# Kernel tuning notes

Hardware: AMD Instinct MI355X
Metric: run time of the kernel (lower is better)

## Reference

```python
import jax, jax.numpy as jnp
import numpy as np

N_NODES = 500_000
N_EDGES = 16_000_000
N_TYPES = 64


def setup_inputs() -> dict:
    key = jax.random.key(0)
    ks = jax.random.split(key, 8)
    voltage = jax.random.normal(ks[0], (N_NODES,), dtype=jnp.float32)
    stimulus = jax.random.normal(ks[1], (N_NODES,), dtype=jnp.float32)
    neuron_type = jax.random.randint(ks[2], (N_NODES,), 0, N_TYPES, dtype=jnp.int64)
    edge_index = jax.random.randint(ks[3], (2, N_EDGES), 0, N_NODES, dtype=jnp.int64)
    w = jax.random.normal(ks[4], (N_EDGES,), dtype=jnp.float32)
    V_i_rest = jax.random.normal(ks[5], (N_NODES,), dtype=jnp.float32)
    # tau must be positive (divisor); shift uniform away from zero
    tau_i = jax.random.uniform(ks[6], (N_NODES,), dtype=jnp.float32) + 0.5
    # multiple_ReLU per-type scale, abs(1 + 0.5*randn) as in the module
    type_params = jnp.abs(1.0 + 0.5 * jax.random.normal(ks[7], (N_TYPES, 1), dtype=jnp.float32))
    return {
        "voltage": voltage,
        "stimulus": stimulus,
        "neuron_type": neuron_type,
        "edge_index": edge_index,
        "w": w,
        "V_i_rest": V_i_rest,
        "tau_i": tau_i,
        "type_params": type_params,
    }


def reference(voltage, stimulus, neuron_type, edge_index, w, V_i_rest, tau_i, type_params):
    # voltage: (N,), edge_index: (2,E), w: (E,), type_params: (T,1)
    v = voltage[:, None]  # (N,1)
    src = edge_index[0]
    dst = edge_index[1]
    # per-edge message: w_e * relu(v_src) * param[type(src)]   -> (E,1)
    edge_msg = w[:, None] * jax.nn.relu(v[src]) * type_params[neuron_type[src]]
    # scatter_add to destination nodes -> (N,1)
    msg = jax.ops.segment_sum(edge_msg, dst, num_segments=v.shape[0])
    # dv/dt = (-v + msg + e + v_rest) / tau
    dv = (-v + msg + stimulus[:, None] + V_i_rest[:, None]) / tau_i[:, None]
    return dv
```

## Files before the change

### kernel.cpp

```cpp
#include <hip/hip_runtime.h>


#define BSHIFT 11
#define BSIZE  2048
#define NBMAX  256
#define GPB    4096
#define EPB    (GPB * 4)
#define EPBP   (EPB + 1024)
#define MAPSZ  (EPBP / 4)
#define SPILL_CAP 131072

__device__ __forceinline__ unsigned pack_rec(float x, int d) {
    return ((__float_as_uint(x) + (unsigned)(BSIZE >> 1)) & ~(unsigned)(BSIZE - 1)) |
           ((unsigned)d & (BSIZE - 1));
}


__global__ void pre_g_kernel(const float* __restrict__ v,
                             const int* __restrict__ ntype,
                             const float* __restrict__ tp,
                             float* __restrict__ g,
                             unsigned* __restrict__ gcur,
                             int n, int nb) {
    int i = blockIdx.x * blockDim.x + threadIdx.x;
    if (i < n) {
        float x = v[i];
        x = x > 0.0f ? x : 0.0f;
        g[i] = x * tp[ntype[i]];
    }
    if (i <= nb) gcur[i] = 0u;
}

__global__ __launch_bounds__(1024, 8)
void scatter_kernel(const int* __restrict__ src,
                    const int* __restrict__ dst,
                    const float* __restrict__ w,
                    const float* __restrict__ g,
                    unsigned* __restrict__ bucketbuf,
                    unsigned* __restrict__ gcur,
                    uint2* __restrict__ spill,
                    int G, int n_edges, int nblk, int nb, int cap) {
    __shared__ unsigned stage[EPBP];
    __shared__ unsigned lstart[NBMAX];
    __shared__ unsigned lcur[NBMAX];
    __shared__ unsigned gposs[NBMAX];
    __shared__ unsigned char qmap[MAPSZ];
    __shared__ unsigned wsum[16];
    int blk = blockIdx.x, tid = threadIdx.x;
    int wid = tid >> 6, lane = tid & 63;
    bool last = (blk == nblk - 1);

    if (tid < NBMAX) lcur[tid] = 0;
    __syncthreads();

    const int4*   s4 = (const int4*)src;
    const int4*   d4 = (const int4*)dst;
    const float4* w4 = (const float4*)w;
    int gstart = blk * GPB;
    int gend = gstart + GPB; if (gend > G) gend = G;
    bool full = (gend - gstart) == GPB;

    int4 dreg[4];
    float4 wreg[4];
    float gv[16];
    if (full) {
        int i0 = gstart + tid;
        int4 dA = d4[i0], dB = d4[i0 + 1024], dC = d4[i0 + 2048], dD = d4[i0 + 3072];
        int4 sA = s4[i0], sB = s4[i0 + 1024], sC = s4[i0 + 2048], sD = s4[i0 + 3072];
        wreg[0] = w4[i0]; wreg[1] = w4[i0 + 1024];
        wreg[2] = w4[i0 + 2048]; wreg[3] = w4[i0 + 3072];
        gv[0]  = g[sA.x]; gv[1]  = g[sA.y]; gv[2]  = g[sA.z]; gv[3]  = g[sA.w];
        gv[4]  = g[sB.x]; gv[5]  = g[sB.y]; gv[6]  = g[sB.z]; gv[7]  = g[sB.w];
        gv[8]  = g[sC.x]; gv[9]  = g[sC.y]; gv[10] = g[sC.z]; gv[11] = g[sC.w];
        gv[12] = g[sD.x]; gv[13] = g[sD.y]; gv[14] = g[sD.z]; gv[15] = g[sD.w];
        dreg[0] = dA; dreg[1] = dB; dreg[2] = dC; dreg[3] = dD;
        atomicAdd(&lcur[((unsigned)dA.x) >> BSHIFT], 1u);
        atomicAdd(&lcur[((unsigned)dA.y) >> BSHIFT], 1u);
        atomicAdd(&lcur[((unsigned)dA.z) >> BSHIFT], 1u);
        atomicAdd(&lcur[((unsigned)dA.w) >> BSHIFT], 1u);
        atomicAdd(&lcur[((unsigned)dB.x) >> BSHIFT], 1u);
        atomicAdd(&lcur[((unsigned)dB.y) >> BSHIFT], 1u);
        atomicAdd(&lcur[((unsigned)dB.z) >> BSHIFT], 1u);
        atomicAdd(&lcur[((unsigned)dB.w) >> BSHIFT], 1u);
        atomicAdd(&lcur[((unsigned)dC.x) >> BSHIFT], 1u);
        atomicAdd(&lcur[((unsigned)dC.y) >> BSHIFT], 1u);
        atomicAdd(&lcur[((unsigned)dC.z) >> BSHIFT], 1u);
        atomicAdd(&lcur[((unsigned)dC.w) >> BSHIFT], 1u);
        atomicAdd(&lcur[((unsigned)dD.x) >> BSHIFT], 1u);
        atomicAdd(&lcur[((unsigned)dD.y) >> BSHIFT], 1u);
        atomicAdd(&lcur[((unsigned)dD.z) >> BSHIFT], 1u);
        atomicAdd(&lcur[((unsigned)dD.w) >> BSHIFT], 1u);
    } else {
        #pragma unroll
        for (int k = 0; k < 4; k++) {
            int i = gstart + tid + k * 1024;
            if (i < gend) {
                int4 d = d4[i];
                dreg[k] = d;
                atomicAdd(&lcur[((unsigned)d.x) >> BSHIFT], 1u);
                atomicAdd(&lcur[((unsigned)d.y) >> BSHIFT], 1u);
                atomicAdd(&lcur[((unsigned)d.z) >> BSHIFT], 1u);
                atomicAdd(&lcur[((unsigned)d.w) >> BSHIFT], 1u);
            }
        }
    }
    if (last) {
        for (int i = G * 4 + tid; i < n_edges; i += 1024)
            atomicAdd(&lcur[((unsigned)dst[i]) >> BSHIFT], 1u);
    }
    __syncthreads();

    unsigned rawc = (tid < NBMAX) ? lcur[tid] : 0u;
    unsigned cntv = (rawc + 3u) & ~3u;
    unsigned inc = cntv;
    #pragma unroll
    for (int o = 1; o < 64; o <<= 1) {
        unsigned t = __shfl_up(inc, o, 64);
        if (lane >= o) inc += t;
    }
    if (lane == 63) wsum[wid] = inc;
    __syncthreads();
    if (tid < 64) {
        unsigned x = (lane < 16) ? wsum[lane] : 0u;
        unsigned xi = x;
        #pragma unroll
        for (int o = 1; o < 16; o <<= 1) {
            unsigned t = __shfl_up(xi, o, 64);
            if (lane >= o) xi += t;
        }
        if (lane < 16) wsum[lane] = xi - x;
    }
    __syncthreads();
    if (tid < NBMAX) {
        unsigned excl = inc - cntv + wsum[wid];
        lstart[tid] = excl;
        lcur[tid] = excl;
    }
    __syncthreads();

    if (full) {
        #pragma unroll
        for (int k = 0; k < 4; k++) {
            float4 wv = wreg[k];
            int4 d = dreg[k];
            unsigned pos;
            pos = atomicAdd(&lcur[((unsigned)d.x) >> BSHIFT], 1u);
            stage[pos] = pack_rec(wv.x * gv[4 * k + 0], d.x);
            pos = atomicAdd(&lcur[((unsigned)d.y) >> BSHIFT], 1u);
            stage[pos] = pack_rec(wv.y * gv[4 * k + 1], d.y);
            pos = atomicAdd(&lcur[((unsigned)d.z) >> BSHIFT], 1u);
            stage[pos] = pack_rec(wv.z * gv[4 * k + 2], d.z);
            pos = atomicAdd(&lcur[((unsigned)d.w) >> BSHIFT], 1u);
            stage[pos] = pack_rec(wv.w * gv[4 * k + 3], d.w);
        }
    } else {
        #pragma unroll
        for (int k = 0; k < 4; k++) {
            int i = gstart + tid + k * 1024;
            if (i < gend) {
                int4 s = s4[i]; float4 wv = w4[i]; int4 d = dreg[k];
                unsigned pos;
                pos = atomicAdd(&lcur[((unsigned)d.x) >> BSHIFT], 1u);
                stage[pos] = pack_rec(wv.x * g[s.x], d.x);
                pos = atomicAdd(&lcur[((unsigned)d.y) >> BSHIFT], 1u);
                stage[pos] = pack_rec(wv.y * g[s.y], d.y);
                pos = atomicAdd(&lcur[((unsigned)d.z) >> BSHIFT], 1u);
                stage[pos] = pack_rec(wv.z * g[s.z], d.z);
                pos = atomicAdd(&lcur[((unsigned)d.w) >> BSHIFT], 1u);
                stage[pos] = pack_rec(wv.w * g[s.w], d.w);
            }
        }
    }
    if (last) {
        for (int i = G * 4 + tid; i < n_edges; i += 1024) {
            int dd = dst[i];
            unsigned b = ((unsigned)dd) >> BSHIFT;
            unsigned pos = atomicAdd(&lcur[b], 1u);
            stage[pos] = pack_rec(w[i] * g[src[i]], dd);
        }
    }
    __syncthreads();

    if (tid < nb) {
        unsigned st   = lstart[tid];
        unsigned end  = lcur[tid];
        unsigned len  = end - st;
        unsigned len4 = (len + 3u) & ~3u;
        unsigned p = 0u;
        if (len) {
            p = atomicAdd(&gcur[tid], len4);
            if (p + len4 > (unsigned)cap) {
                atomicSub(&gcur[tid], len4);
                unsigned sp = atomicAdd(&gcur[nb], len4);
                p = 0x80000000u | sp;
            }
            for (unsigned j = end; j < st + len4; j++)
                stage[j] = j & (unsigned)(BSIZE - 1);
            for (unsigned q = st >> 2; q < (st + len4) >> 2; q++)
                qmap[q] = (unsigned char)tid;
        }
        gposs[tid] = p;
    }
    __syncthreads();

    unsigned total4 = lstart[nb] >> 2;
    const uint4* st4 = (const uint4*)stage;
    for (unsigned q = tid; q < total4; q += 1024) {
        unsigned b = qmap[q];
        unsigned p = gposs[b];
        unsigned roff = (q << 2) - lstart[b];
        if (p & 0x80000000u) {
            unsigned sp = (p & 0x7FFFFFFFu) + roff;
            #pragma unroll
            for (int t = 0; t < 4; t++) {
                if (sp + t < SPILL_CAP) {
                    unsigned u = stage[(q << 2) + t];
                    spill[sp + t] = make_uint2((b << BSHIFT) | (u & (BSIZE - 1u)),
                                               u & ~(unsigned)(BSIZE - 1));
                }
            }
        } else {
            uint4* dp4 = (uint4*)(bucketbuf + (size_t)b * (unsigned)cap + p + roff);
            *dp4 = st4[q];
        }
    }
}

__global__ __launch_bounds__(1024, 2)
void accum_kernel(const unsigned* __restrict__ bucketbuf,
                  const unsigned* __restrict__ gcur,
                  const uint2* __restrict__ spill,
                  const float* __restrict__ v,
                  const float* __restrict__ stim,
                  const float* __restrict__ vrest,
                  const float* __restrict__ tau,
                  float* __restrict__ out,
                  int n_nodes, int nb, int cap) {
    __shared__ float acc[BSIZE];
    int b = blockIdx.x, tid = threadIdx.x;
    acc[tid] = 0.0f;
    acc[tid + 1024] = 0.0f;
    __syncthreads();

    int i0 = (b << BSHIFT) + tid;
    int i1 = i0 + 1024;
    bool ok0 = i0 < n_nodes, ok1 = i1 < n_nodes;
    float v0 = 0.f, s0 = 0.f, r0 = 0.f, t0 = 1.f;
    float v1 = 0.f, s1 = 0.f, r1 = 0.f, t1 = 1.f;
    if (ok0) { v0 = v[i0]; s0 = stim[i0]; r0 = vrest[i0]; t0 = tau[i0]; }
    if (ok1) { v1 = v[i1]; s1 = stim[i1]; r1 = vrest[i1]; t1 = tau[i1]; }

    unsigned cnt = gcur[b];
    if (cnt > (unsigned)cap) cnt = (unsigned)cap;
    const unsigned* base = bucketbuf + (size_t)b * (unsigned)cap;
    const uint4* b4 = (const uint4*)base;
    unsigned nq = cnt >> 2;
    for (unsigned i = tid; i < nq; i += 1024) {
        uint4 u = b4[i];
        atomicAdd(&acc[u.x & (BSIZE - 1u)], __uint_as_float(u.x & ~(unsigned)(BSIZE - 1)));
        atomicAdd(&acc[u.y & (BSIZE - 1u)], __uint_as_float(u.y & ~(unsigned)(BSIZE - 1)));
        atomicAdd(&acc[u.z & (BSIZE - 1u)], __uint_as_float(u.z & ~(unsigned)(BSIZE - 1)));
        atomicAdd(&acc[u.w & (BSIZE - 1u)], __uint_as_float(u.w & ~(unsigned)(BSIZE - 1)));
    }
    for (unsigned i = (nq << 2) + tid; i < cnt; i += 1024) {
        unsigned u = base[i];
        atomicAdd(&acc[u & (BSIZE - 1u)], __uint_as_float(u & ~(unsigned)(BSIZE - 1)));
    }

    unsigned sn = gcur[nb];
    if (sn) {
        if (sn > SPILL_CAP) sn = SPILL_CAP;
        for (unsigned i = tid; i < sn; i += 1024) {
            uint2 e = spill[i];
            if ((int)(e.x >> BSHIFT) == b)
                atomicAdd(&acc[e.x & (BSIZE - 1u)], __uint_as_float(e.y));
        }
    }
    __syncthreads();

    if (ok0) out[i0] = (-v0 + acc[tid] + s0 + r0) / t0;
    if (ok1) out[i1] = (-v1 + acc[tid + 1024] + s1 + r1) / t1;
}


__global__ void node_pre_kernel(const float* __restrict__ v,
                                const int* __restrict__ ntype,
                                const float* __restrict__ tp,
                                float* __restrict__ g,
                                float* __restrict__ msg, int n) {
    int i = blockIdx.x * blockDim.x + threadIdx.x;
    if (i < n) {
        float x = v[i];
        x = x > 0.0f ? x : 0.0f;
        g[i] = x * tp[ntype[i]];
        msg[i] = 0.0f;
    }
}

__global__ void edge_scatter_kernel(const int* __restrict__ src,
                                    const int* __restrict__ dst,
                                    const float* __restrict__ w,
                                    const float* __restrict__ g,
                                    float* __restrict__ msg, int n_vec) {
    int i = blockIdx.x * blockDim.x + threadIdx.x;
    if (i < n_vec) {
        int4 s = ((const int4*)src)[i];
        int4 d = ((const int4*)dst)[i];
        float4 wv = ((const float4*)w)[i];
        atomicAdd(&msg[d.x], wv.x * g[s.x]);
        atomicAdd(&msg[d.y], wv.y * g[s.y]);
        atomicAdd(&msg[d.z], wv.z * g[s.z]);
        atomicAdd(&msg[d.w], wv.w * g[s.w]);
    }
}

__global__ void edge_scatter_tail(const int* __restrict__ src,
                                  const int* __restrict__ dst,
                                  const float* __restrict__ w,
                                  const float* __restrict__ g,
                                  float* __restrict__ msg,
                                  int start, int n_edges) {
    int i = start + blockIdx.x * blockDim.x + threadIdx.x;
    if (i < n_edges) atomicAdd(&msg[dst[i]], w[i] * g[src[i]]);
}

__global__ void node_post_kernel(const float* __restrict__ v,
                                 const float* __restrict__ msg,
                                 const float* __restrict__ stim,
                                 const float* __restrict__ vrest,
                                 const float* __restrict__ tau,
                                 float* __restrict__ out, int n) {
    int i = blockIdx.x * blockDim.x + threadIdx.x;
    if (i < n)
        out[i] = (-v[i] + msg[i] + stim[i] + vrest[i]) / tau[i];
}


extern "C" void kernel_launch(void* const* d_in, const int* in_sizes, int n_in,
                              void* d_out, int out_size, void* d_ws, size_t ws_size,
                              hipStream_t stream) {
    const float* voltage  = (const float*)d_in[0];
    const float* stimulus = (const float*)d_in[1];
    const int*   ntype    = (const int*)d_in[2];
    const int*   edge_idx = (const int*)d_in[3];
    const float* w        = (const float*)d_in[4];
    const float* vrest    = (const float*)d_in[5];
    const float* tau      = (const float*)d_in[6];
    const float* tp       = (const float*)d_in[7];
    float* out = (float*)d_out;

    const int n_nodes = in_sizes[0];
    const int n_edges = in_sizes[4];
    const int* src = edge_idx;
    const int* dst = edge_idx + n_edges;

    const int B = 256;
    const int G = n_edges / 4;
    int nblk = (G + GPB - 1) / GPB;
    if (nblk < 1) nblk = 1;
    const int nb = (n_nodes + BSIZE - 1) / BSIZE;

    auto align256 = [](size_t x) { return (x + 255) & ~(size_t)255; };

    int base_cap = (int)(((long long)n_edges * BSIZE) / (long long)(n_nodes > 0 ? n_nodes : 1));
    const int slacks[3] = {4096, 3072, 2048};
    int cap = 0;
    size_t g_off = 0, gcur_off = 0, spill_off = 0, bb_off = 0, need = (size_t)-1;
    for (int si = 0; si < 3; si++) {
        int c = (base_cap + slacks[si] + 3) & ~3;
        size_t go  = 0;
        size_t gc  = align256(go + (size_t)n_nodes * 4);
        size_t sp  = align256(gc + (size_t)(nb + 1) * 4);
        size_t bb  = align256(sp + (size_t)SPILL_CAP * 8);
        size_t nd  = align256(bb + (size_t)nb * (size_t)c * 4);
        if (nd <= ws_size) {
            cap = c; g_off = go; gcur_off = gc; spill_off = sp; bb_off = bb; need = nd;
            break;
        }
    }

    if (nb < NBMAX && cap > 0 && need <= ws_size) {
        float*    g         = (float*)((char*)d_ws + g_off);
        unsigned* gcur      = (unsigned*)((char*)d_ws + gcur_off);
        uint2*    spill     = (uint2*)((char*)d_ws + spill_off);
        unsigned* bucketbuf = (unsigned*)((char*)d_ws + bb_off);

        pre_g_kernel<<<(n_nodes + B - 1) / B, B, 0, stream>>>(
            voltage, ntype, tp, g, gcur, n_nodes, nb);
        scatter_kernel<<<nblk, 1024, 0, stream>>>(
            src, dst, w, g, bucketbuf, gcur, spill, G, n_edges, nblk, nb, cap);
        accum_kernel<<<nb, 1024, 0, stream>>>(
            bucketbuf, gcur, spill, voltage, stimulus, vrest, tau, out,
            n_nodes, nb, cap);
    } else {
        float* g   = (float*)d_ws;
        float* msg = (float*)d_ws + n_nodes;
        node_pre_kernel<<<(n_nodes + B - 1) / B, B, 0, stream>>>(
            voltage, ntype, tp, g, msg, n_nodes);
        if (G > 0)
            edge_scatter_kernel<<<(G + B - 1) / B, B, 0, stream>>>(
                src, dst, w, g, msg, G);
        if (G * 4 < n_edges) {
            int rem = n_edges - G * 4;
            edge_scatter_tail<<<(rem + B - 1) / B, B, 0, stream>>>(
                src, dst, w, g, msg, G * 4, n_edges);
        }
        node_post_kernel<<<(n_nodes + B - 1) / B, B, 0, stream>>>(
            voltage, msg, stimulus, vrest, tau, out, n_nodes);
    }
}
```

Before: 420.9 us.

## Shrink scatter blocks to 256 threads, pad global bucket cursors, drop padding records

The scatter kernel now runs 256-thread blocks that each handle 768 int4 groups instead of 1024-thread blocks handling 4096. Weight loads move into the placement loop to cut register use, and the global per-bucket cursors are spaced 16 words apart so they do not contend on shared cache lines. Buckets are no longer padded to multiples of 4 with dummy records; partial quads are written element by element instead. This aims for more resident blocks, better latency hiding and less atomic contention. The cost is many more blocks, each issuing global atomics per bucket, which raises total atomic traffic, plus more scalar tail writes.

```diff
diff --git a/kernel.cpp b/kernel.cpp
--- a/kernel.cpp
+++ b/kernel.cpp
@@ -4,10 +4,12 @@
 #define BSHIFT 11
 #define BSIZE  2048
 #define NBMAX  256
-#define GPB    4096
+#define BTH    256
+#define GPB    768
 #define EPB    (GPB * 4)
-#define EPBP   (EPB + 1024)
+#define EPBP   (EPB + 736)
 #define MAPSZ  (EPBP / 4)
+#define GSTRIDE 16
 #define SPILL_CAP 131072
 
 __device__ __forceinline__ unsigned pack_rec(float x, int d) {
@@ -28,10 +30,10 @@
         x = x > 0.0f ? x : 0.0f;
         g[i] = x * tp[ntype[i]];
     }
-    if (i <= nb) gcur[i] = 0u;
-}
-
-__global__ __launch_bounds__(1024, 8)
+    if (i < (nb + 1) * GSTRIDE) gcur[i] = 0u;
+}
+
+__global__ __launch_bounds__(BTH, 8)
 void scatter_kernel(const int* __restrict__ src,
                     const int* __restrict__ dst,
                     const float* __restrict__ w,
@@ -50,7 +52,7 @@
     int wid = tid >> 6, lane = tid & 63;
     bool last = (blk == nblk - 1);
 
-    if (tid < NBMAX) lcur[tid] = 0;
+    lcur[tid] = 0;
     __syncthreads();
 
     const int4*   s4 = (const int4*)src;
@@ -60,20 +62,16 @@
     int gend = gstart + GPB; if (gend > G) gend = G;
     bool full = (gend - gstart) == GPB;
 
-    int4 dreg[4];
-    float4 wreg[4];
-    float gv[16];
+    int4 dreg[3];
+    float gv[12];
     if (full) {
         int i0 = gstart + tid;
-        int4 dA = d4[i0], dB = d4[i0 + 1024], dC = d4[i0 + 2048], dD = d4[i0 + 3072];
-        int4 sA = s4[i0], sB = s4[i0 + 1024], sC = s4[i0 + 2048], sD = s4[i0 + 3072];
-        wreg[0] = w4[i0]; wreg[1] = w4[i0 + 1024];
-        wreg[2] = w4[i0 + 2048]; wreg[3] = w4[i0 + 3072];
-        gv[0]  = g[sA.x]; gv[1]  = g[sA.y]; gv[2]  = g[sA.z]; gv[3]  = g[sA.w];
-        gv[4]  = g[sB.x]; gv[5]  = g[sB.y]; gv[6]  = g[sB.z]; gv[7]  = g[sB.w];
-        gv[8]  = g[sC.x]; gv[9]  = g[sC.y]; gv[10] = g[sC.z]; gv[11] = g[sC.w];
-        gv[12] = g[sD.x]; gv[13] = g[sD.y]; gv[14] = g[sD.z]; gv[15] = g[sD.w];
-        dreg[0] = dA; dreg[1] = dB; dreg[2] = dC; dreg[3] = dD;
+        int4 dA = d4[i0], dB = d4[i0 + BTH], dC = d4[i0 + 2 * BTH];
+        int4 sA = s4[i0], sB = s4[i0 + BTH], sC = s4[i0 + 2 * BTH];
+        gv[0] = g[sA.x]; gv[1] = g[sA.y]; gv[2]  = g[sA.z]; gv[3]  = g[sA.w];
+        gv[4] = g[sB.x]; gv[5] = g[sB.y]; gv[6]  = g[sB.z]; gv[7]  = g[sB.w];
+        gv[8] = g[sC.x]; gv[9] = g[sC.y]; gv[10] = g[sC.z]; gv[11] = g[sC.w];
+        dreg[0] = dA; dreg[1] = dB; dreg[2] = dC;
         atomicAdd(&lcur[((unsigned)dA.x) >> BSHIFT], 1u);
         atomicAdd(&lcur[((unsigned)dA.y) >> BSHIFT], 1u);
         atomicAdd(&lcur[((unsigned)dA.z) >> BSHIFT], 1u);
@@ -86,14 +84,10 @@
         atomicAdd(&lcur[((unsigned)dC.y) >> BSHIFT], 1u);
         atomicAdd(&lcur[((unsigned)dC.z) >> BSHIFT], 1u);
         atomicAdd(&lcur[((unsigned)dC.w) >> BSHIFT], 1u);
-        atomicAdd(&lcur[((unsigned)dD.x) >> BSHIFT], 1u);
-        atomicAdd(&lcur[((unsigned)dD.y) >> BSHIFT], 1u);
-        atomicAdd(&lcur[((unsigned)dD.z) >> BSHIFT], 1u);
-        atomicAdd(&lcur[((unsigned)dD.w) >> BSHIFT], 1u);
     } else {
         #pragma unroll
-        for (int k = 0; k < 4; k++) {
-            int i = gstart + tid + k * 1024;
+        for (int k = 0; k < 3; k++) {
+            int i = gstart + tid + k * BTH;
             if (i < gend) {
                 int4 d = d4[i];
                 dreg[k] = d;
@@ -105,12 +99,12 @@
         }
     }
     if (last) {
-        for (int i = G * 4 + tid; i < n_edges; i += 1024)
+        for (int i = G * 4 + tid; i < n_edges; i += BTH)
             atomicAdd(&lcur[((unsigned)dst[i]) >> BSHIFT], 1u);
     }
     __syncthreads();
 
-    unsigned rawc = (tid < NBMAX) ? lcur[tid] : 0u;
+    unsigned rawc = lcur[tid];
     unsigned cntv = (rawc + 3u) & ~3u;
     unsigned inc = cntv;
     #pragma unroll
@@ -121,17 +115,17 @@
     if (lane == 63) wsum[wid] = inc;
     __syncthreads();
     if (tid < 64) {
-        unsigned x = (lane < 16) ? wsum[lane] : 0u;
+        unsigned x = (lane < 4) ? wsum[lane] : 0u;
         unsigned xi = x;
         #pragma unroll
-        for (int o = 1; o < 16; o <<= 1) {
+        for (int o = 1; o < 4; o <<= 1) {
             unsigned t = __shfl_up(xi, o, 64);
             if (lane >= o) xi += t;
         }
-        if (lane < 16) wsum[lane] = xi - x;
-    }
-    __syncthreads();
-    if (tid < NBMAX) {
+        if (lane < 4) wsum[lane] = xi - x;
+    }
+    __syncthreads();
+    {
         unsigned excl = inc - cntv + wsum[wid];
         lstart[tid] = excl;
         lcur[tid] = excl;
@@ -139,9 +133,10 @@
     __syncthreads();
 
     if (full) {
+        int i0 = gstart + tid;
         #pragma unroll
-        for (int k = 0; k < 4; k++) {
-            float4 wv = wreg[k];
+        for (int k = 0; k < 3; k++) {
+            float4 wv = w4[i0 + k * BTH];
             int4 d = dreg[k];
             unsigned pos;
             pos = atomicAdd(&lcur[((unsigned)d.x) >> BSHIFT], 1u);
@@ -155,8 +150,8 @@
         }
     } else {
         #pragma unroll
-        for (int k = 0; k < 4; k++) {
-            int i = gstart + tid + k * 1024;
+        for (int k = 0; k < 3; k++) {
+            int i = gstart + tid + k * BTH;
             if (i < gend) {
                 int4 s = s4[i]; float4 wv = w4[i]; int4 d = dreg[k];
                 unsigned pos;
@@ -172,7 +167,7 @@
         }
     }
     if (last) {
-        for (int i = G * 4 + tid; i < n_edges; i += 1024) {
+        for (int i = G * 4 + tid; i < n_edges; i += BTH) {
             int dd = dst[i];
             unsigned b = ((unsigned)dd) >> BSHIFT;
             unsigned pos = atomicAdd(&lcur[b], 1u);
@@ -182,21 +177,17 @@
     __syncthreads();
 
     if (tid < nb) {
-        unsigned st   = lstart[tid];
-        unsigned end  = lcur[tid];
-        unsigned len  = end - st;
-        unsigned len4 = (len + 3u) & ~3u;
+        unsigned st  = lstart[tid];
+        unsigned len = lcur[tid] - st;
         unsigned p = 0u;
         if (len) {
-            p = atomicAdd(&gcur[tid], len4);
-            if (p + len4 > (unsigned)cap) {
-                atomicSub(&gcur[tid], len4);
-                unsigned sp = atomicAdd(&gcur[nb], len4);
+            p = atomicAdd(&gcur[tid * GSTRIDE], len);
+            if (p + len > (unsigned)cap) {
+                atomicSub(&gcur[tid * GSTRIDE], len);
+                unsigned sp = atomicAdd(&gcur[nb * GSTRIDE], len);
                 p = 0x80000000u | sp;
             }
-            for (unsigned j = end; j < st + len4; j++)
-                stage[j] = j & (unsigned)(BSIZE - 1);
-            for (unsigned q = st >> 2; q < (st + len4) >> 2; q++)
+            for (unsigned q = st >> 2; q < (st + len + 3u) >> 2; q++)
                 qmap[q] = (unsigned char)tid;
         }
         gposs[tid] = p;
@@ -205,14 +196,16 @@
 
     unsigned total4 = lstart[nb] >> 2;
     const uint4* st4 = (const uint4*)stage;
-    for (unsigned q = tid; q < total4; q += 1024) {
+    for (unsigned q = tid; q < total4; q += BTH) {
         unsigned b = qmap[q];
+        unsigned st = lstart[b];
         unsigned p = gposs[b];
-        unsigned roff = (q << 2) - lstart[b];
+        unsigned roff = (q << 2) - st;
+        unsigned len = lcur[b] - st;
+        unsigned nvalid = len - roff; if (nvalid > 4u) nvalid = 4u;
         if (p & 0x80000000u) {
             unsigned sp = (p & 0x7FFFFFFFu) + roff;
-            #pragma unroll
-            for (int t = 0; t < 4; t++) {
+            for (unsigned t = 0; t < nvalid; t++) {
                 if (sp + t < SPILL_CAP) {
                     unsigned u = stage[(q << 2) + t];
                     spill[sp + t] = make_uint2((b << BSHIFT) | (u & (BSIZE - 1u)),
@@ -220,8 +213,13 @@
                 }
             }
         } else {
-            uint4* dp4 = (uint4*)(bucketbuf + (size_t)b * (unsigned)cap + p + roff);
-            *dp4 = st4[q];
+            unsigned* dp = bucketbuf + (size_t)b * (unsigned)cap + p + roff;
+            if (nvalid == 4u) {
+                *(uint4*)dp = st4[q];
+            } else {
+                for (unsigned t = 0; t < nvalid; t++)
+                    dp[t] = stage[(q << 2) + t];
+            }
         }
     }
 }
@@ -250,7 +248,7 @@
     if (ok0) { v0 = v[i0]; s0 = stim[i0]; r0 = vrest[i0]; t0 = tau[i0]; }
     if (ok1) { v1 = v[i1]; s1 = stim[i1]; r1 = vrest[i1]; t1 = tau[i1]; }
 
-    unsigned cnt = gcur[b];
+    unsigned cnt = gcur[b * GSTRIDE];
     if (cnt > (unsigned)cap) cnt = (unsigned)cap;
     const unsigned* base = bucketbuf + (size_t)b * (unsigned)cap;
     const uint4* b4 = (const uint4*)base;
@@ -267,7 +265,7 @@
         atomicAdd(&acc[u & (BSIZE - 1u)], __uint_as_float(u & ~(unsigned)(BSIZE - 1)));
     }
 
-    unsigned sn = gcur[nb];
+    unsigned sn = gcur[nb * GSTRIDE];
     if (sn) {
         if (sn > SPILL_CAP) sn = SPILL_CAP;
         for (unsigned i = tid; i < sn; i += 1024) {
@@ -370,7 +368,7 @@
         int c = (base_cap + slacks[si] + 3) & ~3;
         size_t go  = 0;
         size_t gc  = align256(go + (size_t)n_nodes * 4);
-        size_t sp  = align256(gc + (size_t)(nb + 1) * 4);
+        size_t sp  = align256(gc + (size_t)(nb + 1) * GSTRIDE * 4);
         size_t bb  = align256(sp + (size_t)SPILL_CAP * 8);
         size_t nd  = align256(bb + (size_t)nb * (size_t)c * 4);
         if (nd <= ws_size) {
@@ -387,7 +385,7 @@
 
         pre_g_kernel<<<(n_nodes + B - 1) / B, B, 0, stream>>>(
             voltage, ntype, tp, g, gcur, n_nodes, nb);
-        scatter_kernel<<<nblk, 1024, 0, stream>>>(
+        scatter_kernel<<<nblk, BTH, 0, stream>>>(
             src, dst, w, g, bucketbuf, gcur, spill, G, n_edges, nblk, nb, cap);
         accum_kernel<<<nb, 1024, 0, stream>>>(
             bucketbuf, gcur, spill, voltage, stimulus, vrest, tau, out,
```

Result: slower. 450.5 us (+7.0%).
